# Kernel tuning notes

Measured on AMD Instinct MI355X. Metric: run time of the kernel, lower is better.

Reference implementation:

```python
import jax, jax.numpy as jnp
import numpy as np

VOCAB, EMB, HID = 1000, 128, 256
B, T = 64, 1024


def setup_inputs() -> dict:
    key = jax.random.key(0)
    k1, k2, k3, k4, k5, k6, k7 = jax.random.split(key, 7)
    loading_lists = jax.random.randint(k1, (B, T), 0, VOCAB)
    lengths = jnp.maximum(jax.random.randint(k2, (B,), 0, T), 1)  # length >= 1 as in env
    s_ih = 1.0 / np.sqrt(HID)
    return {
        "loading_lists": loading_lists,
        "loading_list_lengths": lengths,
        "emb": jax.random.normal(k3, (VOCAB, EMB), dtype=jnp.float32),
        "W_ih": jax.random.uniform(k4, (4 * HID, EMB), minval=-s_ih, maxval=s_ih, dtype=jnp.float32),
        "W_hh": jax.random.uniform(k5, (4 * HID, HID), minval=-s_ih, maxval=s_ih, dtype=jnp.float32),
        "b_ih": jax.random.uniform(k6, (4 * HID,), minval=-s_ih, maxval=s_ih, dtype=jnp.float32),
        "b_hh": jax.random.uniform(k7, (4 * HID,), minval=-s_ih, maxval=s_ih, dtype=jnp.float32),
    }


def reference(loading_lists, loading_list_lengths, emb, W_ih, W_hh, b_ih, b_hh):
    # Embedding lookup: [B, T, E]
    x = emb[loading_lists]
    Bv, Tv, _ = x.shape
    H = W_hh.shape[1]
    # Precompute input projections for all timesteps: [B, T, 4H]
    xproj = jnp.einsum("bte,ge->btg", x, W_ih) + b_ih + b_hh
    xproj_t = jnp.swapaxes(xproj, 0, 1)  # [T, B, 4H]
    lengths = loading_list_lengths

    def step(carry, inp):
        h, c = carry
        xw_t, t = inp
        gates = xw_t + h @ W_hh.T  # [B, 4H]
        i_g, f_g, g_g, o_g = jnp.split(gates, 4, axis=-1)  # torch gate order i,f,g,o
        i_g = jax.nn.sigmoid(i_g)
        f_g = jax.nn.sigmoid(f_g)
        g_g = jnp.tanh(g_g)
        o_g = jax.nn.sigmoid(o_g)
        c_new = f_g * c + i_g * g_g
        h_new = o_g * jnp.tanh(c_new)
        valid = (t < lengths)[:, None]  # freeze state past each sample's length
        h = jnp.where(valid, h_new, h)
        c = jnp.where(valid, c_new, c)
        return (h, c), None

    h0 = jnp.zeros((Bv, H), dtype=x.dtype)
    c0 = jnp.zeros((Bv, H), dtype=x.dtype)
    (h_last, _), _ = jax.lax.scan(step, (h0, c0), (xproj_t, jnp.arange(Tv)))
    return h_last  # [B, H]
```

## Files before the change

### kernel.cpp

```cpp
#include <hip/hip_runtime.h>
#include <math.h>

#define VOCAB 1000
#define EMB   128
#define HID   256
#define G4    1024
#define BATCH 64
#define SEQT  1024
#define KV    92
#define KL    36

typedef unsigned int u32;
typedef _Float16 f16;
typedef __attribute__((ext_vector_type(2))) _Float16 h2v;
union H2U { u32 u; h2v h; unsigned short s[2]; };

#if defined(__has_builtin)
# if __has_builtin(__builtin_amdgcn_fdot2)
#  define HAVE_FDOT2 1
# endif
#endif
__device__ __forceinline__ float fdot2_(u32 a, u32 b, float c) {
    H2U ua, ub; ua.u = a; ub.u = b;
#ifdef HAVE_FDOT2
    return __builtin_amdgcn_fdot2(ua.h, ub.h, c, false);
#else
    return c + (float)ua.h.x * (float)ub.h.x + (float)ua.h.y * (float)ub.h.y;
#endif
}

__device__ __forceinline__ float sigmoidf_(float x) {
    return 1.f / (1.f + __expf(-x));
}
__device__ __forceinline__ float tanhf_(float x) {
    return 1.f - 2.f / (__expf(2.f * x) + 1.f);
}

__global__ __launch_bounds__(1024) void eproj_kernel(
    const float* __restrict__ emb, const float* __restrict__ W_ih,
    const float* __restrict__ b_ih, const float* __restrict__ b_hh,
    float* __restrict__ eproj)
{
    const int v = blockIdx.x;
    const int g = threadIdx.x;
    __shared__ __align__(16) float x_sh[EMB];
    if (g < EMB / 4) {
        ((float4*)x_sh)[g] = ((const float4*)(emb + (size_t)v * EMB))[g];
    }
    __syncthreads();
    const float4* wrow = (const float4*)(W_ih + (size_t)g * EMB);
    float a0 = 0.f, a1 = 0.f, a2 = 0.f, a3 = 0.f;
#pragma unroll
    for (int e4 = 0; e4 < EMB / 4; e4++) {
        float4 wv = wrow[e4];
        float4 xv = ((const float4*)x_sh)[e4];
        a0 += wv.x * xv.x;
        a1 += wv.y * xv.y;
        a2 += wv.z * xv.z;
        a3 += wv.w * xv.w;
    }
    eproj[(size_t)v * G4 + g] = (a0 + a1) + (a2 + a3) + b_ih[g] + b_hh[g];
}

__global__ __launch_bounds__(128) void pack_whh(
    const float* __restrict__ Whh, u32* __restrict__ wvq, u32* __restrict__ wlq)
{
    const int r = blockIdx.x;
    const int m = threadIdx.x;
    H2U u;
    u.h.x = (f16)Whh[(size_t)r * HID + 2 * m];
    u.h.y = (f16)Whh[(size_t)r * HID + 2 * m + 1];
    if (m < KV) {
        wvq[(size_t)(m >> 2) * (G4 * 4) + r * 4 + (m & 3)] = u.u;
    } else {
        const int mm = m - KV;
        wlq[(size_t)(mm >> 2) * (G4 * 4) + r * 4 + (mm & 3)] = u.u;
    }
}

__global__ __launch_bounds__(512, 2) void lstm_single_cu(
    const int* __restrict__ ids, const int* __restrict__ lens,
    const float* __restrict__ eproj,
    const u32* __restrict__ wvq, const u32* __restrict__ wlq,
    float* __restrict__ out)
{
    const int b   = blockIdx.x;
    const int tau = threadIdx.x;
    const int rA  = tau;
    const int rB  = 512 + tau;

    __shared__ u32 wl_sh[KL / 4 * G4 * 4];
    __shared__ u32 h2_sh[2][HID / 2];
    __shared__ float gs_f[HID], gs_o[HID];

    {
        const uint4* src = (const uint4*)wlq;
        uint4*       dst = (uint4*)wl_sh;
#pragma unroll
        for (int t = 0; t < (KL / 4) * G4 / 512; t++)
            dst[t * 512 + tau] = src[t * 512 + tau];
    }
    if (tau < HID / 2) h2_sh[0][tau] = 0u;

    u32 wA[KV], wB[KV];
#pragma unroll
    for (int q = 0; q < KV / 4; q++) {
        uint4 ta = ((const uint4*)wvq)[q * G4 + rA];
        uint4 tb = ((const uint4*)wvq)[q * G4 + rB];
        wA[4 * q + 0] = ta.x; wA[4 * q + 1] = ta.y;
        wA[4 * q + 2] = ta.z; wA[4 * q + 3] = ta.w;
        wB[4 * q + 0] = tb.x; wB[4 * q + 1] = tb.y;
        wB[4 * q + 2] = tb.z; wB[4 * q + 3] = tb.w;
    }

    const int len = lens[b];
    const int* idr = ids + (size_t)b * SEQT;
    float c = 0.f, hf = 0.f;

    const float* e0 = eproj + (size_t)idr[0] * G4;
    float xA = e0[rA], xB = e0[rB];

    __syncthreads();

    for (int t = 0; t < len; t++) {
        const int nt = (t + 1 < len) ? t + 1 : len - 1;
        const float* en = eproj + (size_t)idr[nt] * G4;
        const float nA = en[rA], nB = en[rB];

        const int p = t & 1;
        const uint4* hb4 = (const uint4*)h2_sh[p];
        float aA = xA, aB = xB;

#pragma unroll
        for (int q = 0; q < KV / 4; q++) {
            uint4 h4 = hb4[q];
            aA = fdot2_(wA[4 * q + 0], h4.x, aA);
            aB = fdot2_(wB[4 * q + 0], h4.x, aB);
            aA = fdot2_(wA[4 * q + 1], h4.y, aA);
            aB = fdot2_(wB[4 * q + 1], h4.y, aB);
            aA = fdot2_(wA[4 * q + 2], h4.z, aA);
            aB = fdot2_(wB[4 * q + 2], h4.z, aB);
            aA = fdot2_(wA[4 * q + 3], h4.w, aA);
            aB = fdot2_(wB[4 * q + 3], h4.w, aB);
        }
#pragma unroll
        for (int q = 0; q < KL / 4; q++) {
            uint4 h4 = hb4[KV / 4 + q];
            uint4 tA = ((const uint4*)wl_sh)[q * G4 + rA];
            uint4 tB = ((const uint4*)wl_sh)[q * G4 + rB];
            aA = fdot2_(tA.x, h4.x, aA);
            aB = fdot2_(tB.x, h4.x, aB);
            aA = fdot2_(tA.y, h4.y, aA);
            aB = fdot2_(tB.y, h4.y, aB);
            aA = fdot2_(tA.z, h4.z, aA);
            aB = fdot2_(tB.z, h4.z, aB);
            aA = fdot2_(tA.w, h4.w, aA);
            aB = fdot2_(tB.w, h4.w, aB);
        }

        if (tau >= HID) {
            gs_f[tau - HID] = aA;
            gs_o[tau - HID] = aB;
        }
        __syncthreads();

        if (tau < HID) {
            float ig = sigmoidf_(aA);
            float gg = tanhf_(aB);
            float fg = sigmoidf_(gs_f[tau]);
            float og = sigmoidf_(gs_o[tau]);
            c = fg * c + ig * gg;
            hf = og * tanhf_(c);
            H2U hv; hv.h.x = (f16)hf; hv.h.y = (f16)0.f;
            ((unsigned short*)h2_sh[p ^ 1])[tau] = hv.s[0];
        }
        xA = nA; xB = nB;
        __syncthreads();
    }

    if (tau < HID) out[(size_t)b * HID + tau] = hf;
}

__global__ __launch_bounds__(1024, 1) void lstm_fallback(
    const int* __restrict__ ids, const int* __restrict__ lens,
    const float* __restrict__ emb, const float* __restrict__ W_ih,
    const float* __restrict__ b_ih, const float* __restrict__ b_hh,
    const float* __restrict__ W_hh, float* __restrict__ out)
{
    const int b = blockIdx.x;
    const int t = threadIdx.x;

    __shared__ __align__(16) float h_sh[HID];
    __shared__ __align__(16) float c_sh[HID];
    __shared__ __align__(16) float gates[G4];
    __shared__ __align__(16) float x_sh[EMB];

    float wih[EMB];
    {
        const float4* wr = (const float4*)(W_ih + (size_t)t * EMB);
#pragma unroll
        for (int e4 = 0; e4 < EMB / 4; e4++) {
            float4 wv = wr[e4];
            wih[4 * e4 + 0] = wv.x;
            wih[4 * e4 + 1] = wv.y;
            wih[4 * e4 + 2] = wv.z;
            wih[4 * e4 + 3] = wv.w;
        }
    }
    float bias = b_ih[t] + b_hh[t];

    const int len = lens[b];
    const int* ids_row = ids + (size_t)b * SEQT;
    if (t < HID) { h_sh[t] = 0.f; c_sh[t] = 0.f; }
    __syncthreads();

    for (int step = 0; step < len; step++) {
        int id = ids_row[step];
        if (t < EMB / 4) {
            ((float4*)x_sh)[t] = ((const float4*)(emb + (size_t)id * EMB))[t];
        }
        __syncthreads();
        float a0 = bias, a1 = 0.f, a2 = 0.f, a3 = 0.f;
#pragma unroll
        for (int e4 = 0; e4 < EMB / 4; e4++) {
            float4 xv = ((const float4*)x_sh)[e4];
            a0 += wih[4 * e4 + 0] * xv.x;
            a1 += wih[4 * e4 + 1] * xv.y;
            a2 += wih[4 * e4 + 2] * xv.z;
            a3 += wih[4 * e4 + 3] * xv.w;
        }
        float acc = (a0 + a1) + (a2 + a3);

        const float* wrow = W_hh + (size_t)t * HID;
        a0 = acc; a1 = 0.f; a2 = 0.f; a3 = 0.f;
        for (int k4 = 0; k4 < HID / 4; k4++) {
            float4 hv = ((const float4*)h_sh)[k4];
            float4 wv = ((const float4*)wrow)[k4];
            a0 += wv.x * hv.x;
            a1 += wv.y * hv.y;
            a2 += wv.z * hv.z;
            a3 += wv.w * hv.w;
        }
        gates[t] = (a0 + a1) + (a2 + a3);
        __syncthreads();

        if (t < HID) {
            float ig = sigmoidf_(gates[t]);
            float fg = sigmoidf_(gates[HID + t]);
            float gg = tanhf_(gates[2 * HID + t]);
            float og = sigmoidf_(gates[3 * HID + t]);
            float cc = fg * c_sh[t] + ig * gg;
            c_sh[t] = cc;
            h_sh[t] = og * tanhf_(cc);
        }
        __syncthreads();
    }
    if (t < HID) out[(size_t)b * HID + t] = h_sh[t];
}

extern "C" void kernel_launch(void* const* d_in, const int* in_sizes, int n_in,
                              void* d_out, int out_size, void* d_ws, size_t ws_size,
                              hipStream_t stream) {
    const int*   ids  = (const int*)d_in[0];
    const int*   lens = (const int*)d_in[1];
    const float* emb  = (const float*)d_in[2];
    const float* Wih  = (const float*)d_in[3];
    const float* Whh  = (const float*)d_in[4];
    const float* bih  = (const float*)d_in[5];
    const float* bhh  = (const float*)d_in[6];
    float* out = (float*)d_out;

    const size_t ep_bytes = (size_t)VOCAB * G4 * sizeof(float);
    const size_t wv_off   = ep_bytes;
    const size_t wv_bytes = (size_t)(KV / 4) * G4 * 4 * sizeof(u32);
    const size_t wl_off   = wv_off + wv_bytes;
    const size_t wl_bytes = (size_t)(KL / 4) * G4 * 4 * sizeof(u32);

    if (ws_size >= wl_off + wl_bytes) {
        float* eproj = (float*)d_ws;
        u32*   wvp   = (u32*)((char*)d_ws + wv_off);
        u32*   wlp   = (u32*)((char*)d_ws + wl_off);
        eproj_kernel<<<VOCAB, 1024, 0, stream>>>(emb, Wih, bih, bhh, eproj);
        pack_whh<<<G4, 128, 0, stream>>>(Whh, wvp, wlp);
        lstm_single_cu<<<BATCH, 512, 0, stream>>>(ids, lens, eproj, wvp, wlp, out);
    } else {
        lstm_fallback<<<BATCH, 1024, 0, stream>>>(
            ids, lens, emb, Wih, bih, bhh, Whh, out);
    }
}
```

Measured before the change: 1.768 ms.

## Map one gate row per thread with 1024-thread blocks and cache token ids

The recurrent kernel goes from 512 threads that each compute two gate rows to 1024 threads that each compute one. This halves the per-thread dot-product chain and the register-resident weight footprint on the serial critical path. Three of the four gate quarters now go through shared memory for the elementwise LSTM update, instead of two. Token ids are staged into shared memory so the next-step embedding-projection lookup no longer reads the id from global memory. The risks are tighter register limits from the new launch bounds and more shared-memory traffic per step.

After: 2.121 ms. 20.0% more time.

```diff
diff --git a/kernel.cpp b/kernel.cpp
--- a/kernel.cpp
+++ b/kernel.cpp
@@ -78,7 +78,7 @@
     }
 }
 
-__global__ __launch_bounds__(512, 2) void lstm_single_cu(
+__global__ __launch_bounds__(1024, 4) void lstm_single_cu(
     const int* __restrict__ ids, const int* __restrict__ lens,
     const float* __restrict__ eproj,
     const u32* __restrict__ wvq, const u32* __restrict__ wlq,
@@ -86,95 +86,84 @@
 {
     const int b   = blockIdx.x;
     const int tau = threadIdx.x;
-    const int rA  = tau;
-    const int rB  = 512 + tau;
-
-    __shared__ u32 wl_sh[KL / 4 * G4 * 4];
-    __shared__ u32 h2_sh[2][HID / 2];
-    __shared__ float gs_f[HID], gs_o[HID];
+
+    __shared__ u32   wl_sh[KL / 4 * G4 * 4];
+    __shared__ u32   h2_sh[2][HID / 2];
+    __shared__ float gs_f[HID], gs_g[HID], gs_o[HID];
+    __shared__ int   id_sh[SEQT];
+
+    const int* idr = ids + (size_t)b * SEQT;
+    id_sh[tau] = idr[tau];
+    if (tau < HID / 2) h2_sh[0][tau] = 0u;
 
     {
         const uint4* src = (const uint4*)wlq;
         uint4*       dst = (uint4*)wl_sh;
 #pragma unroll
-        for (int t = 0; t < (KL / 4) * G4 / 512; t++)
-            dst[t * 512 + tau] = src[t * 512 + tau];
-    }
-    if (tau < HID / 2) h2_sh[0][tau] = 0u;
-
-    u32 wA[KV], wB[KV];
+        for (int t = 0; t < (KL / 4) * G4 / 1024; t++)
+            dst[t * 1024 + tau] = src[t * 1024 + tau];
+    }
+
+    u32 wA[KV];
 #pragma unroll
     for (int q = 0; q < KV / 4; q++) {
-        uint4 ta = ((const uint4*)wvq)[q * G4 + rA];
-        uint4 tb = ((const uint4*)wvq)[q * G4 + rB];
+        uint4 ta = ((const uint4*)wvq)[q * G4 + tau];
         wA[4 * q + 0] = ta.x; wA[4 * q + 1] = ta.y;
         wA[4 * q + 2] = ta.z; wA[4 * q + 3] = ta.w;
-        wB[4 * q + 0] = tb.x; wB[4 * q + 1] = tb.y;
-        wB[4 * q + 2] = tb.z; wB[4 * q + 3] = tb.w;
     }
 
     const int len = lens[b];
-    const int* idr = ids + (size_t)b * SEQT;
+    const int g2  = tau >> 8;
+    const int u   = tau & (HID - 1);
     float c = 0.f, hf = 0.f;
 
-    const float* e0 = eproj + (size_t)idr[0] * G4;
-    float xA = e0[rA], xB = e0[rB];
+    float xA = eproj[(size_t)idr[0] * G4 + tau];
 
     __syncthreads();
 
     for (int t = 0; t < len; t++) {
         const int nt = (t + 1 < len) ? t + 1 : len - 1;
-        const float* en = eproj + (size_t)idr[nt] * G4;
-        const float nA = en[rA], nB = en[rB];
+        const int nid = id_sh[nt];
+        const float nA = eproj[(size_t)nid * G4 + tau];
 
         const int p = t & 1;
         const uint4* hb4 = (const uint4*)h2_sh[p];
-        float aA = xA, aB = xB;
+        float aA = xA;
 
 #pragma unroll
         for (int q = 0; q < KV / 4; q++) {
             uint4 h4 = hb4[q];
             aA = fdot2_(wA[4 * q + 0], h4.x, aA);
-            aB = fdot2_(wB[4 * q + 0], h4.x, aB);
             aA = fdot2_(wA[4 * q + 1], h4.y, aA);
-            aB = fdot2_(wB[4 * q + 1], h4.y, aB);
             aA = fdot2_(wA[4 * q + 2], h4.z, aA);
-            aB = fdot2_(wB[4 * q + 2], h4.z, aB);
             aA = fdot2_(wA[4 * q + 3], h4.w, aA);
-            aB = fdot2_(wB[4 * q + 3], h4.w, aB);
         }
 #pragma unroll
         for (int q = 0; q < KL / 4; q++) {
             uint4 h4 = hb4[KV / 4 + q];
-            uint4 tA = ((const uint4*)wl_sh)[q * G4 + rA];
-            uint4 tB = ((const uint4*)wl_sh)[q * G4 + rB];
+            uint4 tA = ((const uint4*)wl_sh)[q * G4 + tau];
             aA = fdot2_(tA.x, h4.x, aA);
-            aB = fdot2_(tB.x, h4.x, aB);
             aA = fdot2_(tA.y, h4.y, aA);
-            aB = fdot2_(tB.y, h4.y, aB);
             aA = fdot2_(tA.z, h4.z, aA);
-            aB = fdot2_(tB.z, h4.z, aB);
             aA = fdot2_(tA.w, h4.w, aA);
-            aB = fdot2_(tB.w, h4.w, aB);
-        }
-
-        if (tau >= HID) {
-            gs_f[tau - HID] = aA;
-            gs_o[tau - HID] = aB;
-        }
-        __syncthreads();
-
-        if (tau < HID) {
+        }
+
+        if (g2 == 1)      gs_f[u] = aA;
+        else if (g2 == 2) gs_g[u] = aA;
+        else if (g2 == 3) gs_o[u] = aA;
+        __syncthreads();
+
+        if (g2 == 0) {
             float ig = sigmoidf_(aA);
-            float gg = tanhf_(aB);
-            float fg = sigmoidf_(gs_f[tau]);
-            float og = sigmoidf_(gs_o[tau]);
+            float fg = sigmoidf_(gs_f[u]);
+            float gg = tanhf_(gs_g[u]);
+            float og = sigmoidf_(gs_o[u]);
             c = fg * c + ig * gg;
             hf = og * tanhf_(c);
             H2U hv; hv.h.x = (f16)hf; hv.h.y = (f16)0.f;
-            ((unsigned short*)h2_sh[p ^ 1])[tau] = hv.s[0];
-        }
-        xA = nA; xB = nB;
+            ((unsigned short*)h2_sh[p ^ 1])[u] = hv.s[0];
+        }
+        xA = nA;
         __syncthreads();
     }
 
@@ -282,7 +271,7 @@
         u32*   wlp   = (u32*)((char*)d_ws + wl_off);
         eproj_kernel<<<VOCAB, 1024, 0, stream>>>(emb, Wih, bih, bhh, eproj);
         pack_whh<<<G4, 128, 0, stream>>>(Whh, wvp, wlp);
-        lstm_single_cu<<<BATCH, 512, 0, stream>>>(ids, lens, eproj, wvp, wlp, out);
+        lstm_single_cu<<<BATCH, 1024, 0, stream>>>(ids, lens, eproj, wvp, wlp, out);
     } else {
         lstm_fallback<<<BATCH, 1024, 0, stream>>>(
             ids, lens, emb, Wih, bih, bhh, Whh, out);
```

## Broadcast hidden state via readlane, cache token ids in LDS, split gate activations

Applied to the files above, without the earlier changes.

Each wave now loads the hidden-state vector once into two registers per lane and broadcasts each element with readlane, replacing repeated uint4 LDS broadcast reads inside the dot-product loops. Token ids for the sequence are staged in shared memory so the next-step prefetch avoids a dependent global load. Gate nonlinearities are split so upper threads apply the sigmoid to f/o before the barrier, which moves work off the post-barrier critical path. Readlane produces scalar values that may need SGPR-to-VGPR moves, and the readlane count grows with K.

New measurement: 2.014 ms. 14.0% more time.

```diff
diff --git a/kernel.cpp b/kernel.cpp
--- a/kernel.cpp
+++ b/kernel.cpp
@@ -27,6 +27,10 @@
 #else
     return c + (float)ua.h.x * (float)ub.h.x + (float)ua.h.y * (float)ub.h.y;
 #endif
+}
+
+__device__ __forceinline__ u32 rl_(u32 hv0, u32 hv1, int idx) {
+    return (u32)__builtin_amdgcn_readlane((int)(idx < 64 ? hv0 : hv1), idx & 63);
 }
 
 __device__ __forceinline__ float sigmoidf_(float x) {
@@ -88,10 +92,16 @@
     const int tau = threadIdx.x;
     const int rA  = tau;
     const int rB  = 512 + tau;
-
-    __shared__ u32 wl_sh[KL / 4 * G4 * 4];
-    __shared__ u32 h2_sh[2][HID / 2];
+    const int ln  = tau & 63;
+
+    __shared__ u32   wl_sh[KL / 4 * G4 * 4];
+    __shared__ u32   h2_sh[2][HID / 2];
     __shared__ float gs_f[HID], gs_o[HID];
+    __shared__ int   id_sh[SEQT];
+
+    const int* idr = ids + (size_t)b * SEQT;
+    ((int2*)id_sh)[tau] = ((const int2*)idr)[tau];
+    if (tau < HID / 2) h2_sh[0][tau] = 0u;
 
     {
         const uint4* src = (const uint4*)wlq;
@@ -100,7 +110,6 @@
         for (int t = 0; t < (KL / 4) * G4 / 512; t++)
             dst[t * 512 + tau] = src[t * 512 + tau];
     }
-    if (tau < HID / 2) h2_sh[0][tau] = 0u;
 
     u32 wA[KV], wB[KV];
 #pragma unroll
@@ -114,7 +123,6 @@
     }
 
     const int len = lens[b];
-    const int* idr = ids + (size_t)b * SEQT;
     float c = 0.f, hf = 0.f;
 
     const float* e0 = eproj + (size_t)idr[0] * G4;
@@ -124,53 +132,61 @@
 
     for (int t = 0; t < len; t++) {
         const int nt = (t + 1 < len) ? t + 1 : len - 1;
-        const float* en = eproj + (size_t)idr[nt] * G4;
+        const int nid = id_sh[nt];
+        const float* en = eproj + (size_t)nid * G4;
         const float nA = en[rA], nB = en[rB];
 
         const int p = t & 1;
-        const uint4* hb4 = (const uint4*)h2_sh[p];
+        const u32 hv0 = h2_sh[p][ln];
+        const u32 hv1 = h2_sh[p][64 + ln];
         float aA = xA, aB = xB;
 
 #pragma unroll
         for (int q = 0; q < KV / 4; q++) {
-            uint4 h4 = hb4[q];
-            aA = fdot2_(wA[4 * q + 0], h4.x, aA);
-            aB = fdot2_(wB[4 * q + 0], h4.x, aB);
-            aA = fdot2_(wA[4 * q + 1], h4.y, aA);
-            aB = fdot2_(wB[4 * q + 1], h4.y, aB);
-            aA = fdot2_(wA[4 * q + 2], h4.z, aA);
-            aB = fdot2_(wB[4 * q + 2], h4.z, aB);
-            aA = fdot2_(wA[4 * q + 3], h4.w, aA);
-            aB = fdot2_(wB[4 * q + 3], h4.w, aB);
+            u32 h0 = rl_(hv0, hv1, 4 * q + 0);
+            u32 h1 = rl_(hv0, hv1, 4 * q + 1);
+            u32 h2 = rl_(hv0, hv1, 4 * q + 2);
+            u32 h3 = rl_(hv0, hv1, 4 * q + 3);
+            aA = fdot2_(wA[4 * q + 0], h0, aA);
+            aB = fdot2_(wB[4 * q + 0], h0, aB);
+            aA = fdot2_(wA[4 * q + 1], h1, aA);
+            aB = fdot2_(wB[4 * q + 1], h1, aB);
+            aA = fdot2_(wA[4 * q + 2], h2, aA);
+            aB = fdot2_(wB[4 * q + 2], h2, aB);
+            aA = fdot2_(wA[4 * q + 3], h3, aA);
+            aB = fdot2_(wB[4 * q + 3], h3, aB);
         }
 #pragma unroll
         for (int q = 0; q < KL / 4; q++) {
-            uint4 h4 = hb4[KV / 4 + q];
+            u32 h0 = rl_(hv0, hv1, KV + 4 * q + 0);
+            u32 h1 = rl_(hv0, hv1, KV + 4 * q + 1);
+            u32 h2 = rl_(hv0, hv1, KV + 4 * q + 2);
+            u32 h3 = rl_(hv0, hv1, KV + 4 * q + 3);
             uint4 tA = ((const uint4*)wl_sh)[q * G4 + rA];
             uint4 tB = ((const uint4*)wl_sh)[q * G4 + rB];
-            aA = fdot2_(tA.x, h4.x, aA);
-            aB = fdot2_(tB.x, h4.x, aB);
-            aA = fdot2_(tA.y, h4.y, aA);
-            aB = fdot2_(tB.y, h4.y, aB);
-            aA = fdot2_(tA.z, h4.z, aA);
-            aB = fdot2_(tB.z, h4.z, aB);
-            aA = fdot2_(tA.w, h4.w, aA);
-            aB = fdot2_(tB.w, h4.w, aB);
-        }
-
+            aA = fdot2_(tA.x, h0, aA);
+            aB = fdot2_(tB.x, h0, aB);
+            aA = fdot2_(tA.y, h1, aA);
+            aB = fdot2_(tB.y, h1, aB);
+            aA = fdot2_(tA.z, h2, aA);
+            aB = fdot2_(tB.z, h2, aB);
+            aA = fdot2_(tA.w, h3, aA);
+            aB = fdot2_(tB.w, h3, aB);
+        }
+
+        float ig = 0.f, gg = 0.f;
         if (tau >= HID) {
-            gs_f[tau - HID] = aA;
-            gs_o[tau - HID] = aB;
+            gs_f[tau - HID] = sigmoidf_(aA);
+            gs_o[tau - HID] = sigmoidf_(aB);
+        } else {
+            ig = sigmoidf_(aA);
+            gg = tanhf_(aB);
         }
         __syncthreads();
 
         if (tau < HID) {
-            float ig = sigmoidf_(aA);
-            float gg = tanhf_(aB);
-            float fg = sigmoidf_(gs_f[tau]);
-            float og = sigmoidf_(gs_o[tau]);
-            c = fg * c + ig * gg;
-            hf = og * tanhf_(c);
+            c  = gs_f[tau] * c + ig * gg;
+            hf = gs_o[tau] * tanhf_(c);
             H2U hv; hv.h.x = (f16)hf; hv.h.y = (f16)0.f;
             ((unsigned short*)h2_sh[p ^ 1])[tau] = hv.s[0];
         }
```
